# Kernel optimization log

Hardware: AMD Instinct MI355X
Metric: run time of the kernel (lower is better)

The kernel has to match this reference:

```python
import jax, jax.numpy as jnp
import numpy as np

TOP_K = 2
NUM_EXPERTS = 64
AUX_COEF = 0.01


def setup_inputs() -> dict:
    key = jax.random.key(0)
    kx, kw = jax.random.split(key)
    B, S, D, E = 4, 4096, 2048, NUM_EXPERTS
    x = jax.random.normal(kx, (B, S, D), dtype=jnp.float32)
    # nn.Linear default init ~ U(-1/sqrt(D), 1/sqrt(D))
    W = jax.random.uniform(kw, (E, D), dtype=jnp.float32,
                           minval=-1.0 / np.sqrt(D), maxval=1.0 / np.sqrt(D))
    return {"x": x, "W": W}


def reference(x, W):
    B, S, D = x.shape
    E = W.shape[0]
    # router projection (no bias)
    logits = jnp.einsum('bsd,ed->bse', x, W)          # [B,S,E]
    probs = jax.nn.softmax(logits, axis=-1)           # [B,S,E]
    top_k_gates, top_k_indices = jax.lax.top_k(probs, TOP_K)  # [B,S,K]
    top_k_gates = top_k_gates / (jnp.sum(top_k_gates, axis=-1, keepdims=True) + 1e-9)
    # aux loss: fraction of routed slots per expert (one-hot mean) x mean router prob
    total_slots = B * S * TOP_K
    counts = jnp.zeros((E,), dtype=jnp.float32).at[top_k_indices.reshape(-1)].add(1.0)
    avg_tokens_per_expert = counts / total_slots      # == one_hot(idx).mean(dims 0,1,2)
    avg_router_prob = jnp.mean(probs, axis=(0, 1))    # [E]
    aux_loss = AUX_COEF * E * jnp.sum(avg_tokens_per_expert * avg_router_prob)
    return top_k_indices, top_k_gates, aux_loss
```

## Files before the change

kernel.cpp:

```cpp
#include <hip/hip_runtime.h>
#include <math.h>

#define NTOK 16384
#define DDIM 2048
#define NEXP 64
#define TMB  64
#define NBLK (NTOK / TMB)
#define NCHH 16
#define NSH  32

typedef _Float16 half8v __attribute__((ext_vector_type(8)));
typedef float    f32x4  __attribute__((ext_vector_type(4)));

#define MFMA16(a, b, c) __builtin_amdgcn_mfma_f32_16x16x32_f16((a), (b), (c), 0, 0, 0)

__global__ __launch_bounds__(256) void prep_kernel(const float* __restrict__ W,
                                                   _Float16* __restrict__ Wh,
                                                   _Float16* __restrict__ Wl,
                                                   float* __restrict__ accg) {
    int idx = blockIdx.x * 256 + threadIdx.x;
    int e  = idx >> 8;
    int k0 = (idx & 255) << 3;
    const float* wp = W + (size_t)e * DDIM + k0;
    float4 w0 = *(const float4*)wp;
    float4 w1 = *(const float4*)(wp + 4);
    half8v h, l;
    h[0] = (_Float16)w0.x; l[0] = (_Float16)(w0.x - (float)h[0]);
    h[1] = (_Float16)w0.y; l[1] = (_Float16)(w0.y - (float)h[1]);
    h[2] = (_Float16)w0.z; l[2] = (_Float16)(w0.z - (float)h[2]);
    h[3] = (_Float16)w0.w; l[3] = (_Float16)(w0.w - (float)h[3]);
    h[4] = (_Float16)w1.x; l[4] = (_Float16)(w1.x - (float)h[4]);
    h[5] = (_Float16)w1.y; l[5] = (_Float16)(w1.y - (float)h[5]);
    h[6] = (_Float16)w1.z; l[6] = (_Float16)(w1.z - (float)h[6]);
    h[7] = (_Float16)w1.w; l[7] = (_Float16)(w1.w - (float)h[7]);
    int S = k0 >> 5, nb = e >> 4, nl = e & 15, q = (k0 >> 3) & 3;
    size_t off = (size_t)S * 2048 + nb * 512 + q * 128 + nl * 8;
    *(half8v*)&Wh[off] = h;
    *(half8v*)&Wl[off] = l;
    if (idx < 128) accg[idx] = 0.0f;
}

__device__ __forceinline__ void cvt8(float4 a, float4 b, half8v& h, half8v& l) {
    h[0]=(_Float16)a.x; l[0]=(_Float16)(a.x-(float)h[0]);
    h[1]=(_Float16)a.y; l[1]=(_Float16)(a.y-(float)h[1]);
    h[2]=(_Float16)a.z; l[2]=(_Float16)(a.z-(float)h[2]);
    h[3]=(_Float16)a.w; l[3]=(_Float16)(a.w-(float)h[3]);
    h[4]=(_Float16)b.x; l[4]=(_Float16)(b.x-(float)h[4]);
    h[5]=(_Float16)b.y; l[5]=(_Float16)(b.y-(float)h[5]);
    h[6]=(_Float16)b.z; l[6]=(_Float16)(b.z-(float)h[6]);
    h[7]=(_Float16)b.w; l[7]=(_Float16)(b.w-(float)h[7]);
}

__global__ __launch_bounds__(512, 1) void router_kernel(
    const float* __restrict__ x, const _Float16* __restrict__ Wh,
    const _Float16* __restrict__ Wl, float* __restrict__ accg,
    float* __restrict__ out)
{
    __shared__ __align__(16) _Float16 Ah[2][2][4096];
    __shared__ __align__(16) _Float16 Al[2][2][4096];
    __shared__ float lgt[TMB][NEXP + 1];
    __shared__ float pacc[4][64][16];
    __shared__ float cnt[NEXP];

    const int tid  = threadIdx.x;
    const int lane = tid & 63;
    const int wv   = __builtin_amdgcn_readfirstlane(tid >> 6);
    const int eb   = wv & 3;
    const int kh   = wv >> 2;
    const int m0   = blockIdx.x * TMB;

    if (tid < NEXP) cnt[tid] = 0.0f;

    const int st   = tid & 255;
    const int r    = st >> 2;
    const int c0l  = (st & 3) * 16;
    const int tile = r >> 4, tok = r & 15;
    const int S0 = c0l >> 5,       q0 = (c0l >> 3) & 3;
    const int S1 = (c0l+8) >> 5,   q1 = ((c0l+8) >> 3) & 3;
    const int g0 = S0*64 + q0*16 + tok,  g1 = S1*64 + q1*16 + tok;
    const int off0 = tile*1024 + (g0 ^ ((g0>>4)&7)) * 8;
    const int off1 = tile*1024 + (g1 ^ ((g1>>4)&7)) * 8;

    const float* gx = x + (size_t)(m0 + r) * DDIM + kh * 1024 + c0l;

    const int gr1 = 64 + lane;
    const int rd0 = (lane ^ ((lane>>4)&7)) * 8;
    const int rd1 = (gr1 ^ ((gr1>>4)&7)) * 8;

    const _Float16* whp = Wh + (size_t)kh * 65536 + eb * 512 + lane * 8;
    const _Float16* wlp = Wl + (size_t)kh * 65536 + eb * 512 + lane * 8;

    f32x4 acc0 = {0.f,0.f,0.f,0.f}, acc1 = {0.f,0.f,0.f,0.f};
    f32x4 acc2 = {0.f,0.f,0.f,0.f}, acc3 = {0.f,0.f,0.f,0.f};

    float4 xa0 = *(const float4*)(gx +  0), xa1 = *(const float4*)(gx +  4);
    float4 xa2 = *(const float4*)(gx +  8), xa3 = *(const float4*)(gx + 12);
    float4 xb0 = *(const float4*)(gx + 64), xb1 = *(const float4*)(gx + 68);
    float4 xb2 = *(const float4*)(gx + 72), xb3 = *(const float4*)(gx + 76);
    half8v wh0 = *(const half8v*)(whp);
    half8v wh1 = *(const half8v*)(whp + 2048);
    half8v wh2 = *(const half8v*)(whp + 4096);
    half8v wh3 = *(const half8v*)(whp + 6144);
    half8v wl0 = *(const half8v*)(wlp);
    half8v wl1 = *(const half8v*)(wlp + 2048);
    half8v wl2 = *(const half8v*)(wlp + 4096);
    half8v wl3 = *(const half8v*)(wlp + 6144);

#define CHUNK(ch, X0, X1, X2, X3, P, WHA, WLA, WHB, WLB)                    \
    {                                                                        \
        half8v h_, l_;                                                       \
        cvt8(X0, X1, h_, l_);                                                \
        *(half8v*)&Ah[kh][P][off0] = h_;  *(half8v*)&Al[kh][P][off0] = l_;   \
        cvt8(X2, X3, h_, l_);                                                \
        *(half8v*)&Ah[kh][P][off1] = h_;  *(half8v*)&Al[kh][P][off1] = l_;   \
        const int cf = ((ch) + 2 < NCHH) ? (ch) + 2 : 0;                     \
        X0 = *(const float4*)(gx + cf * 64 +  0);                            \
        X1 = *(const float4*)(gx + cf * 64 +  4);                            \
        X2 = *(const float4*)(gx + cf * 64 +  8);                            \
        X3 = *(const float4*)(gx + cf * 64 + 12);                            \
        asm volatile("s_waitcnt lgkmcnt(0)" ::: "memory");                   \
        __builtin_amdgcn_s_barrier();                                        \
        {                                                     \
            half8v a0h = *(const half8v*)&Ah[kh][P][   0 + rd0];             \
            half8v a0l = *(const half8v*)&Al[kh][P][   0 + rd0];             \
            half8v a1h = *(const half8v*)&Ah[kh][P][1024 + rd0];             \
            half8v a1l = *(const half8v*)&Al[kh][P][1024 + rd0];             \
            half8v a2h = *(const half8v*)&Ah[kh][P][2048 + rd0];             \
            half8v a2l = *(const half8v*)&Al[kh][P][2048 + rd0];             \
            half8v a3h = *(const half8v*)&Ah[kh][P][3072 + rd0];             \
            half8v a3l = *(const half8v*)&Al[kh][P][3072 + rd0];             \
            half8v bh = WHA, bl = WLA;                                       \
            const int SgN = (2 * (ch) + 4) & (NSH - 1);                      \
            WHA = *(const half8v*)(whp + (size_t)SgN * 2048);                \
            WLA = *(const half8v*)(wlp + (size_t)SgN * 2048);                \
            acc0 = MFMA16(a0l, bh, acc0);                                    \
            acc0 = MFMA16(a0h, bl, acc0);                                    \
            acc0 = MFMA16(a0h, bh, acc0);                                    \
            acc1 = MFMA16(a1l, bh, acc1);                                    \
            acc1 = MFMA16(a1h, bl, acc1);                                    \
            acc1 = MFMA16(a1h, bh, acc1);                                    \
            acc2 = MFMA16(a2l, bh, acc2);                                    \
            acc2 = MFMA16(a2h, bl, acc2);                                    \
            acc2 = MFMA16(a2h, bh, acc2);                                    \
            acc3 = MFMA16(a3l, bh, acc3);                                    \
            acc3 = MFMA16(a3h, bl, acc3);                                    \
            acc3 = MFMA16(a3h, bh, acc3);                                    \
        }                                                                    \
        {                                                   \
            half8v a0h = *(const half8v*)&Ah[kh][P][   0 + rd1];             \
            half8v a0l = *(const half8v*)&Al[kh][P][   0 + rd1];             \
            half8v a1h = *(const half8v*)&Ah[kh][P][1024 + rd1];             \
            half8v a1l = *(const half8v*)&Al[kh][P][1024 + rd1];             \
            half8v a2h = *(const half8v*)&Ah[kh][P][2048 + rd1];             \
            half8v a2l = *(const half8v*)&Al[kh][P][2048 + rd1];             \
            half8v a3h = *(const half8v*)&Ah[kh][P][3072 + rd1];             \
            half8v a3l = *(const half8v*)&Al[kh][P][3072 + rd1];             \
            half8v bh = WHB, bl = WLB;                                       \
            const int SgN = (2 * (ch) + 5) & (NSH - 1);                      \
            WHB = *(const half8v*)(whp + (size_t)SgN * 2048);                \
            WLB = *(const half8v*)(wlp + (size_t)SgN * 2048);                \
            acc0 = MFMA16(a0l, bh, acc0);                                    \
            acc0 = MFMA16(a0h, bl, acc0);                                    \
            acc0 = MFMA16(a0h, bh, acc0);                                    \
            acc1 = MFMA16(a1l, bh, acc1);                                    \
            acc1 = MFMA16(a1h, bl, acc1);                                    \
            acc1 = MFMA16(a1h, bh, acc1);                                    \
            acc2 = MFMA16(a2l, bh, acc2);                                    \
            acc2 = MFMA16(a2h, bl, acc2);                                    \
            acc2 = MFMA16(a2h, bh, acc2);                                    \
            acc3 = MFMA16(a3l, bh, acc3);                                    \
            acc3 = MFMA16(a3h, bl, acc3);                                    \
            acc3 = MFMA16(a3h, bh, acc3);                                    \
        }                                                                    \
        asm volatile("s_waitcnt lgkmcnt(0)" ::: "memory");                   \
        __builtin_amdgcn_s_barrier();                                        \
    }

    for (int cb = 0; cb < NCHH; cb += 2) {
        CHUNK(cb + 0, xa0, xa1, xa2, xa3, 0, wh0, wl0, wh1, wl1);
        CHUNK(cb + 1, xb0, xb1, xb2, xb3, 1, wh2, wl2, wh3, wl3);
    }
#undef CHUNK

    if (kh == 1) {
        #pragma unroll
        for (int rr = 0; rr < 4; ++rr) {
            pacc[eb][lane][ 0 + rr] = acc0[rr];
            pacc[eb][lane][ 4 + rr] = acc1[rr];
            pacc[eb][lane][ 8 + rr] = acc2[rr];
            pacc[eb][lane][12 + rr] = acc3[rr];
        }
    }
    __syncthreads();

    if (kh == 0) {
        const int qr = lane >> 4;
        const int nl = lane & 15;
        #pragma unroll
        for (int rr = 0; rr < 4; ++rr) {
            const int mm = qr * 4 + rr;
            lgt[ 0 + mm][eb * 16 + nl] = acc0[rr] + pacc[eb][lane][ 0 + rr];
            lgt[16 + mm][eb * 16 + nl] = acc1[rr] + pacc[eb][lane][ 4 + rr];
            lgt[32 + mm][eb * 16 + nl] = acc2[rr] + pacc[eb][lane][ 8 + rr];
            lgt[48 + mm][eb * 16 + nl] = acc3[rr] + pacc[eb][lane][12 + rr];
        }
    }
    __syncthreads();

    {
        const int m = tid >> 3;
        const int j = tid & 7;
        float l[8];
        #pragma unroll
        for (int i = 0; i < 8; ++i) l[i] = lgt[m][j * 8 + i];

        float mx = l[0];
        #pragma unroll
        for (int i = 1; i < 8; ++i) mx = fmaxf(mx, l[i]);
        #pragma unroll
        for (int off = 1; off < 8; off <<= 1) mx = fmaxf(mx, __shfl_xor(mx, off, 8));

        float ev[8];
        float zs = 0.f;
        float v1 = -INFINITY, v2 = -INFINITY;
        int i1 = 0, i2 = 0;
        #pragma unroll
        for (int i = 0; i < 8; ++i) {
            ev[i] = __expf(l[i] - mx);
            zs += ev[i];
            int e = j * 8 + i;
            if (l[i] > v1)      { v2 = v1; i2 = i1; v1 = l[i]; i1 = e; }
            else if (l[i] > v2) { v2 = l[i]; i2 = e; }
        }
        #pragma unroll
        for (int off = 1; off < 8; off <<= 1) zs += __shfl_xor(zs, off, 8);

        #pragma unroll
        for (int off = 1; off < 8; off <<= 1) {
            float ov1 = __shfl_xor(v1, off, 8);
            int   oi1 = __shfl_xor(i1, off, 8);
            float ov2 = __shfl_xor(v2, off, 8);
            int   oi2 = __shfl_xor(i2, off, 8);
            bool afirst = (v1 > ov1) || (v1 == ov1 && i1 < oi1);
            if (afirst) {
                bool t = (v2 > ov1) || (v2 == ov1 && i2 < oi1);
                v2 = t ? v2 : ov1;
                i2 = t ? i2 : oi1;
            } else {
                bool t = (ov2 > v1) || (ov2 == v1 && oi2 < i1);
                v2 = t ? ov2 : v1;
                i2 = t ? oi2 : i1;
                v1 = ov1;
                i1 = oi1;
            }
        }

        const float invz = 1.0f / zs;
        if (j == 0) {
            float p1 = invz;
            float p2 = __expf(v2 - mx) * invz;
            float sden = p1 + p2 + 1e-9f;
            int tokg = m0 + m;
            out[tokg * 2 + 0] = (float)i1;
            out[tokg * 2 + 1] = (float)i2;
            out[32768 + tokg * 2 + 0] = p1 / sden;
            out[32768 + tokg * 2 + 1] = p2 / sden;
            atomicAdd(&cnt[i1], 1.0f);
            atomicAdd(&cnt[i2], 1.0f);
        }

        #pragma unroll
        for (int i = 0; i < 8; ++i) lgt[m][j * 8 + i] = ev[i] * invz;
    }
    __syncthreads();

    if (tid < NEXP) {
        atomicAdd(&accg[tid], cnt[tid]);
    } else if (tid < 128) {
        int e = tid - 64;
        float s = 0.f;
        #pragma unroll
        for (int t = 0; t < TMB; ++t) s += lgt[t][e];
        atomicAdd(&accg[64 + e], s);
    }
}

__global__ void finalize_kernel(const float* __restrict__ accg,
                                float* __restrict__ out)
{
    int t = threadIdx.x;
    float c = accg[t];
    float p = accg[64 + t];
    float term = (c / (float)(NTOK * 2)) * (p / (float)NTOK);
    #pragma unroll
    for (int off = 1; off < 64; off <<= 1) term += __shfl_xor(term, off, 64);
    if (t == 0) out[65536] = 0.01f * (float)NEXP * term;
}

extern "C" void kernel_launch(void* const* d_in, const int* in_sizes, int n_in,
                              void* d_out, int out_size, void* d_ws, size_t ws_size,
                              hipStream_t stream) {
    const float* x = (const float*)d_in[0];
    const float* W = (const float*)d_in[1];
    float* out  = (float*)d_out;
    float* accg = (float*)d_ws;
    _Float16* Wh = (_Float16*)(accg + 128);
    _Float16* Wl = Wh + (size_t)DDIM * NEXP;

    prep_kernel<<<64, 256, 0, stream>>>(W, Wh, Wl, accg);
    router_kernel<<<NBLK, 512, 0, stream>>>(x, Wh, Wl, accg, out);
    finalize_kernel<<<1, 64, 0, stream>>>(accg, out);
}
```

Before: 213.4 us.

## Split router into K-split GEMM kernel and separate softmax/top-k kernel

```diff
diff --git a/kernel.cpp b/kernel.cpp
--- a/kernel.cpp
+++ b/kernel.cpp
@@ -5,7 +5,6 @@
 #define DDIM 2048
 #define NEXP 64
 #define TMB  64
-#define NBLK (NTOK / TMB)
 #define NCHH 16
 #define NSH  32
 
@@ -51,29 +50,22 @@
     h[7]=(_Float16)b.w; l[7]=(_Float16)(b.w-(float)h[7]);
 }
 
-__global__ __launch_bounds__(512, 1) void router_kernel(
+__global__ __launch_bounds__(256, 2) void gemm_kernel(
     const float* __restrict__ x, const _Float16* __restrict__ Wh,
-    const _Float16* __restrict__ Wl, float* __restrict__ accg,
-    float* __restrict__ out)
+    const _Float16* __restrict__ Wl, float* __restrict__ P)
 {
-    __shared__ __align__(16) _Float16 Ah[2][2][4096];
-    __shared__ __align__(16) _Float16 Al[2][2][4096];
-    __shared__ float lgt[TMB][NEXP + 1];
-    __shared__ float pacc[4][64][16];
-    __shared__ float cnt[NEXP];
+    __shared__ __align__(16) _Float16 Ah[2][4096];
+    __shared__ __align__(16) _Float16 Al[2][4096];
 
     const int tid  = threadIdx.x;
     const int lane = tid & 63;
     const int wv   = __builtin_amdgcn_readfirstlane(tid >> 6);
-    const int eb   = wv & 3;
-    const int kh   = wv >> 2;
-    const int m0   = blockIdx.x * TMB;
-
-    if (tid < NEXP) cnt[tid] = 0.0f;
-
-    const int st   = tid & 255;
-    const int r    = st >> 2;
-    const int c0l  = (st & 3) * 16;
+    const int tb   = blockIdx.x >> 1;
+    const int kh   = blockIdx.x & 1;
+    const int m0   = tb * TMB;
+
+    const int r    = tid >> 2;
+    const int c0l  = (tid & 3) * 16;
     const int tile = r >> 4, tok = r & 15;
     const int S0 = c0l >> 5,       q0 = (c0l >> 3) & 3;
     const int S1 = (c0l+8) >> 5,   q1 = ((c0l+8) >> 3) & 3;
@@ -87,8 +79,8 @@
     const int rd0 = (lane ^ ((lane>>4)&7)) * 8;
     const int rd1 = (gr1 ^ ((gr1>>4)&7)) * 8;
 
-    const _Float16* whp = Wh + (size_t)kh * 65536 + eb * 512 + lane * 8;
-    const _Float16* wlp = Wl + (size_t)kh * 65536 + eb * 512 + lane * 8;
+    const _Float16* whp = Wh + (size_t)kh * 65536 + wv * 512 + lane * 8;
+    const _Float16* wlp = Wl + (size_t)kh * 65536 + wv * 512 + lane * 8;
 
     f32x4 acc0 = {0.f,0.f,0.f,0.f}, acc1 = {0.f,0.f,0.f,0.f};
     f32x4 acc2 = {0.f,0.f,0.f,0.f}, acc3 = {0.f,0.f,0.f,0.f};
@@ -106,13 +98,13 @@
     half8v wl2 = *(const half8v*)(wlp + 4096);
     half8v wl3 = *(const half8v*)(wlp + 6144);
 
-#define CHUNK(ch, X0, X1, X2, X3, P, WHA, WLA, WHB, WLB)                    \
+#define CHUNK(ch, X0, X1, X2, X3, PB, WHA, WLA, WHB, WLB)                   \
     {                                                                        \
         half8v h_, l_;                                                       \
         cvt8(X0, X1, h_, l_);                                                \
-        *(half8v*)&Ah[kh][P][off0] = h_;  *(half8v*)&Al[kh][P][off0] = l_;   \
+        *(half8v*)&Ah[PB][off0] = h_;  *(half8v*)&Al[PB][off0] = l_;         \
         cvt8(X2, X3, h_, l_);                                                \
-        *(half8v*)&Ah[kh][P][off1] = h_;  *(half8v*)&Al[kh][P][off1] = l_;   \
+        *(half8v*)&Ah[PB][off1] = h_;  *(half8v*)&Al[PB][off1] = l_;         \
         const int cf = ((ch) + 2 < NCHH) ? (ch) + 2 : 0;                     \
         X0 = *(const float4*)(gx + cf * 64 +  0);                            \
         X1 = *(const float4*)(gx + cf * 64 +  4);                            \
@@ -121,14 +113,14 @@
         asm volatile("s_waitcnt lgkmcnt(0)" ::: "memory");                   \
         __builtin_amdgcn_s_barrier();                                        \
         {                                                     \
-            half8v a0h = *(const half8v*)&Ah[kh][P][   0 + rd0];             \
-            half8v a0l = *(const half8v*)&Al[kh][P][   0 + rd0];             \
-            half8v a1h = *(const half8v*)&Ah[kh][P][1024 + rd0];             \
-            half8v a1l = *(const half8v*)&Al[kh][P][1024 + rd0];             \
-            half8v a2h = *(const half8v*)&Ah[kh][P][2048 + rd0];             \
-            half8v a2l = *(const half8v*)&Al[kh][P][2048 + rd0];             \
-            half8v a3h = *(const half8v*)&Ah[kh][P][3072 + rd0];             \
-            half8v a3l = *(const half8v*)&Al[kh][P][3072 + rd0];             \
+            half8v a0h = *(const half8v*)&Ah[PB][   0 + rd0];                \
+            half8v a0l = *(const half8v*)&Al[PB][   0 + rd0];                \
+            half8v a1h = *(const half8v*)&Ah[PB][1024 + rd0];                \
+            half8v a1l = *(const half8v*)&Al[PB][1024 + rd0];                \
+            half8v a2h = *(const half8v*)&Ah[PB][2048 + rd0];                \
+            half8v a2l = *(const half8v*)&Al[PB][2048 + rd0];                \
+            half8v a3h = *(const half8v*)&Ah[PB][3072 + rd0];                \
+            half8v a3l = *(const half8v*)&Al[PB][3072 + rd0];                \
             half8v bh = WHA, bl = WLA;                                       \
             const int SgN = (2 * (ch) + 4) & (NSH - 1);                      \
             WHA = *(const half8v*)(whp + (size_t)SgN * 2048);                \
@@ -147,14 +139,14 @@
             acc3 = MFMA16(a3h, bh, acc3);                                    \
         }                                                                    \
         {                                                   \
-            half8v a0h = *(const half8v*)&Ah[kh][P][   0 + rd1];             \
-            half8v a0l = *(const half8v*)&Al[kh][P][   0 + rd1];             \
-            half8v a1h = *(const half8v*)&Ah[kh][P][1024 + rd1];             \
-            half8v a1l = *(const half8v*)&Al[kh][P][1024 + rd1];             \
-            half8v a2h = *(const half8v*)&Ah[kh][P][2048 + rd1];             \
-            half8v a2l = *(const half8v*)&Al[kh][P][2048 + rd1];             \
-            half8v a3h = *(const half8v*)&Ah[kh][P][3072 + rd1];             \
-            half8v a3l = *(const half8v*)&Al[kh][P][3072 + rd1];             \
+            half8v a0h = *(const half8v*)&Ah[PB][   0 + rd1];                \
+            half8v a0l = *(const half8v*)&Al[PB][   0 + rd1];                \
+            half8v a1h = *(const half8v*)&Ah[PB][1024 + rd1];                \
+            half8v a1l = *(const half8v*)&Al[PB][1024 + rd1];                \
+            half8v a2h = *(const half8v*)&Ah[PB][2048 + rd1];                \
+            half8v a2l = *(const half8v*)&Al[PB][2048 + rd1];                \
+            half8v a3h = *(const half8v*)&Ah[PB][3072 + rd1];                \
+            half8v a3l = *(const half8v*)&Al[PB][3072 + rd1];                \
             half8v bh = WHB, bl = WLB;                                       \
             const int SgN = (2 * (ch) + 5) & (NSH - 1);                      \
             WHB = *(const half8v*)(whp + (size_t)SgN * 2048);                \
@@ -182,96 +174,99 @@
     }
 #undef CHUNK
 
-    if (kh == 1) {
+    {
+        const int qr = lane >> 4;
+        const int nl = lane & 15;
+        float* gp = P + (size_t)kh * NTOK * NEXP
+                      + (size_t)(m0 + qr * 4) * NEXP + wv * 16 + nl;
         #pragma unroll
         for (int rr = 0; rr < 4; ++rr) {
-            pacc[eb][lane][ 0 + rr] = acc0[rr];
-            pacc[eb][lane][ 4 + rr] = acc1[rr];
-            pacc[eb][lane][ 8 + rr] = acc2[rr];
-            pacc[eb][lane][12 + rr] = acc3[rr];
+            gp[(      rr) * NEXP] = acc0[rr];
+            gp[(16  + rr) * NEXP] = acc1[rr];
+            gp[(32  + rr) * NEXP] = acc2[rr];
+            gp[(48  + rr) * NEXP] = acc3[rr];
         }
     }
+}
+
+__global__ __launch_bounds__(256) void softmax_kernel(
+    const float* __restrict__ P, float* __restrict__ accg,
+    float* __restrict__ out)
+{
+    __shared__ float prb[32][NEXP + 1];
+    __shared__ float cnt[NEXP];
+
+    const int tid = threadIdx.x;
+    const int m0  = blockIdx.x * 32;
+    if (tid < NEXP) cnt[tid] = 0.0f;
     __syncthreads();
 
-    if (kh == 0) {
-        const int qr = lane >> 4;
-        const int nl = lane & 15;
-        #pragma unroll
-        for (int rr = 0; rr < 4; ++rr) {
-            const int mm = qr * 4 + rr;
-            lgt[ 0 + mm][eb * 16 + nl] = acc0[rr] + pacc[eb][lane][ 0 + rr];
-            lgt[16 + mm][eb * 16 + nl] = acc1[rr] + pacc[eb][lane][ 4 + rr];
-            lgt[32 + mm][eb * 16 + nl] = acc2[rr] + pacc[eb][lane][ 8 + rr];
-            lgt[48 + mm][eb * 16 + nl] = acc3[rr] + pacc[eb][lane][12 + rr];
+    const int m = tid >> 3;
+    const int j = tid & 7;
+    const float* pa = P + (size_t)(m0 + m) * NEXP + j * 8;
+    const float* pb = pa + (size_t)NTOK * NEXP;
+    float4 a0 = *(const float4*)pa,       a1 = *(const float4*)(pa + 4);
+    float4 b0 = *(const float4*)pb,       b1 = *(const float4*)(pb + 4);
+    float l[8] = { a0.x + b0.x, a0.y + b0.y, a0.z + b0.z, a0.w + b0.w,
+                   a1.x + b1.x, a1.y + b1.y, a1.z + b1.z, a1.w + b1.w };
+
+    float mx = l[0];
+    #pragma unroll
+    for (int i = 1; i < 8; ++i) mx = fmaxf(mx, l[i]);
+    #pragma unroll
+    for (int off = 1; off < 8; off <<= 1) mx = fmaxf(mx, __shfl_xor(mx, off, 8));
+
+    float ev[8];
+    float zs = 0.f;
+    float v1 = -INFINITY, v2 = -INFINITY;
+    int i1 = 0, i2 = 0;
+    #pragma unroll
+    for (int i = 0; i < 8; ++i) {
+        ev[i] = __expf(l[i] - mx);
+        zs += ev[i];
+        int e = j * 8 + i;
+        if (l[i] > v1)      { v2 = v1; i2 = i1; v1 = l[i]; i1 = e; }
+        else if (l[i] > v2) { v2 = l[i]; i2 = e; }
+    }
+    #pragma unroll
+    for (int off = 1; off < 8; off <<= 1) zs += __shfl_xor(zs, off, 8);
+
+    #pragma unroll
+    for (int off = 1; off < 8; off <<= 1) {
+        float ov1 = __shfl_xor(v1, off, 8);
+        int   oi1 = __shfl_xor(i1, off, 8);
+        float ov2 = __shfl_xor(v2, off, 8);
+        int   oi2 = __shfl_xor(i2, off, 8);
+        bool afirst = (v1 > ov1) || (v1 == ov1 && i1 < oi1);
+        if (afirst) {
+            bool t = (v2 > ov1) || (v2 == ov1 && i2 < oi1);
+            v2 = t ? v2 : ov1;
+            i2 = t ? i2 : oi1;
+        } else {
+            bool t = (ov2 > v1) || (ov2 == v1 && oi2 < i1);
+            v2 = t ? ov2 : v1;
+            i2 = t ? oi2 : i1;
+            v1 = ov1;
+            i1 = oi1;
         }
     }
-    __syncthreads();
-
-    {
-        const int m = tid >> 3;
-        const int j = tid & 7;
-        float l[8];
-        #pragma unroll
-        for (int i = 0; i < 8; ++i) l[i] = lgt[m][j * 8 + i];
-
-        float mx = l[0];
-        #pragma unroll
-        for (int i = 1; i < 8; ++i) mx = fmaxf(mx, l[i]);
-        #pragma unroll
-        for (int off = 1; off < 8; off <<= 1) mx = fmaxf(mx, __shfl_xor(mx, off, 8));
-
-        float ev[8];
-        float zs = 0.f;
-        float v1 = -INFINITY, v2 = -INFINITY;
-        int i1 = 0, i2 = 0;
-        #pragma unroll
-        for (int i = 0; i < 8; ++i) {
-            ev[i] = __expf(l[i] - mx);
-            zs += ev[i];
-            int e = j * 8 + i;
-            if (l[i] > v1)      { v2 = v1; i2 = i1; v1 = l[i]; i1 = e; }
-            else if (l[i] > v2) { v2 = l[i]; i2 = e; }
-        }
-        #pragma unroll
-        for (int off = 1; off < 8; off <<= 1) zs += __shfl_xor(zs, off, 8);
-
-        #pragma unroll
-        for (int off = 1; off < 8; off <<= 1) {
-            float ov1 = __shfl_xor(v1, off, 8);
-            int   oi1 = __shfl_xor(i1, off, 8);
-            float ov2 = __shfl_xor(v2, off, 8);
-            int   oi2 = __shfl_xor(i2, off, 8);
-            bool afirst = (v1 > ov1) || (v1 == ov1 && i1 < oi1);
-            if (afirst) {
-                bool t = (v2 > ov1) || (v2 == ov1 && i2 < oi1);
-                v2 = t ? v2 : ov1;
-                i2 = t ? i2 : oi1;
-            } else {
-                bool t = (ov2 > v1) || (ov2 == v1 && oi2 < i1);
-                v2 = t ? ov2 : v1;
-                i2 = t ? oi2 : i1;
-                v1 = ov1;
-                i1 = oi1;
-            }
-        }
-
-        const float invz = 1.0f / zs;
-        if (j == 0) {
-            float p1 = invz;
-            float p2 = __expf(v2 - mx) * invz;
-            float sden = p1 + p2 + 1e-9f;
-            int tokg = m0 + m;
-            out[tokg * 2 + 0] = (float)i1;
-            out[tokg * 2 + 1] = (float)i2;
-            out[32768 + tokg * 2 + 0] = p1 / sden;
-            out[32768 + tokg * 2 + 1] = p2 / sden;
-            atomicAdd(&cnt[i1], 1.0f);
-            atomicAdd(&cnt[i2], 1.0f);
-        }
-
-        #pragma unroll
-        for (int i = 0; i < 8; ++i) lgt[m][j * 8 + i] = ev[i] * invz;
-    }
+
+    const float invz = 1.0f / zs;
+    if (j == 0) {
+        float p1 = invz;
+        float p2 = __expf(v2 - mx) * invz;
+        float sden = p1 + p2 + 1e-9f;
+        int tokg = m0 + m;
+        out[tokg * 2 + 0] = (float)i1;
+        out[tokg * 2 + 1] = (float)i2;
+        out[32768 + tokg * 2 + 0] = p1 / sden;
+        out[32768 + tokg * 2 + 1] = p2 / sden;
+        atomicAdd(&cnt[i1], 1.0f);
+        atomicAdd(&cnt[i2], 1.0f);
+    }
+
+    #pragma unroll
+    for (int i = 0; i < 8; ++i) prb[m][j * 8 + i] = ev[i] * invz;
     __syncthreads();
 
     if (tid < NEXP) {
@@ -280,7 +275,7 @@
         int e = tid - 64;
         float s = 0.f;
         #pragma unroll
-        for (int t = 0; t < TMB; ++t) s += lgt[t][e];
+        for (int t = 0; t < 32; ++t) s += prb[t][e];
         atomicAdd(&accg[64 + e], s);
     }
 }
@@ -306,8 +301,10 @@
     float* accg = (float*)d_ws;
     _Float16* Wh = (_Float16*)(accg + 128);
     _Float16* Wl = Wh + (size_t)DDIM * NEXP;
+    float* P    = (float*)(Wl + (size_t)DDIM * NEXP);
 
     prep_kernel<<<64, 256, 0, stream>>>(W, Wh, Wl, accg);
-    router_kernel<<<NBLK, 512, 0, stream>>>(x, Wh, Wl, accg, out);
+    gemm_kernel<<<512, 256, 0, stream>>>(x, Wh, Wl, P);
+    softmax_kernel<<<512, 256, 0, stream>>>(P, accg, out);
     finalize_kernel<<<1, 64, 0, stream>>>(accg, out);
 }
```

New measurement: 219.8 us. 3.0% more time.
